# Kernel tuning notes

Hardware: AMD Instinct MI355X
Metric: run time of the kernel (lower is better)

## Reference

```python
import jax, jax.numpy as jnp
import numpy as np
from jax import lax
from jax.scipy.special import logsumexp

NUM_BINS = 1001          # num_bins
K = 127                  # num_quantized_bins = 2**(8-1) - 1 (signed int8, non-narrow)
HALF = NUM_BINS // 2     # 500
EPS = 1e-4               # smoothing_eps
NEG = -1e30              # mask value for logsumexp


def setup_inputs() -> dict:
    key = jax.random.key(0)
    x = jax.random.normal(key, (8, 4096, 1024), dtype=jnp.float32)
    return {"x": x}


def _smooth_logits(v, valid, L):
    # Faithful to smooth_normalize_distribution: hist += eps*is_zeros - eps1*n_nonzeros
    is_zero = valid & (v == 0)
    n_zeros = jnp.sum(is_zero).astype(jnp.float32)
    n_nz = L.astype(jnp.float32) - n_zeros
    eps1 = EPS * n_zeros / jnp.maximum(n_nz, 1.0)
    logits = v + EPS * is_zero.astype(jnp.float32) - eps1 * n_nz
    return logits, n_nz


def reference(x):
    absmax = jnp.max(jnp.abs(x))
    edges = jnp.linspace(-absmax, absmax, NUM_BINS + 1)           # hist_edges, len 1002
    counts, _ = jnp.histogram(x.ravel(), bins=edges)
    hist = lax.stop_gradient(counts.astype(jnp.float32))          # torch.histc(...).int()
    csum = jnp.concatenate([jnp.zeros(1, jnp.float32), jnp.cumsum(hist)])  # exclusive prefix
    total = csum[-1]
    hist_pad = jnp.concatenate([hist, jnp.zeros(NUM_BINS, jnp.float32)])
    k = jnp.arange(NUM_BINS)

    def per_candidate(i):
        start = HALF - i
        stop = HALF + i + 1
        L = 2 * i + 1                          # length of sliced histogram
        valid = k < L
        sliced = lax.dynamic_slice(hist_pad, (start,), (NUM_BINS,))  # first L entries valid
        left = csum[start]                     # sum(hist[:start])
        right = total - csum[stop]             # sum(hist[stop:])
        p = sliced.at[0].add(left).at[L - 1].add(right)
        m = L // K                             # num_merged_bins
        seg = jnp.minimum(k // m, K - 1)       # merged-bin id per position (remainder -> last)
        seg_v = jnp.where(valid, seg, K)       # dump invalid into extra segment
        qb = jax.ops.segment_sum(jnp.where(valid, sliced, 0.0), seg_v, num_segments=K + 1)[:K]
        nz = valid & (sliced != 0)
        # norm for bin j counts nonzeros in its range; last bin uses stop=-1 (excludes k=L-1)
        cnt_mask = nz & (k != L - 1)
        norms = jax.ops.segment_sum(cnt_mask.astype(jnp.float32), seg_v, num_segments=K + 1)[:K]
        nk = norms[seg]
        qbk = qb[seg]
        # q[start:stop] = qb[j]/norm where norm != 0; k=L-1 never assigned; q[sliced==0]=0
        q = jnp.where(nz & (k != L - 1) & (nk > 0), qbk / jnp.maximum(nk, 1.0), 0.0)

        p_log, _ = _smooth_logits(p, valid, L)
        q_log, n_nz_q = _smooth_logits(q, valid, L)
        lZp = logsumexp(jnp.where(valid, p_log, NEG))
        lZq = logsumexp(jnp.where(valid, q_log, NEG))
        lp = p_log - lZp
        lq = q_log - lZq
        probs = jnp.where(valid, jnp.exp(lp), 0.0)
        kl = jnp.sum(probs * (lp - lq) * valid)
        kl = jnp.where(n_nz_q > 0, kl, jnp.inf)  # q all-zero -> divergence = inf
        return edges[stop], kl

    ivals = jnp.arange(K // 2, HALF + 1)        # i = 63 .. 500 (438 candidates)
    thresholds, divergence = jax.vmap(per_candidate)(ivals)
    return thresholds[jnp.argmin(divergence)]
```

## Files before the change

### kernel.cpp

```cpp
#include <hip/hip_runtime.h>
#include <math.h>

#define NBINS 1001
#define KQ 127
#define HALFB 500
#define SEPS 1e-4f
#define NCAND 438
#define IMIN 63
#define PMAXN 2048

typedef float vfloat4 __attribute__((ext_vector_type(4)));

static __device__ __forceinline__ vfloat4 ntload4(const vfloat4* p) {
    return __builtin_nontemporal_load(p);
}


static __device__ __forceinline__ float edge_at(int j, float stepv, float negabs) {
    return __fadd_rn(__fmul_rn((float)j, stepv), negabs);
}

static __device__ __forceinline__ void blockSum2(double& a, double& b, double* s8) {
    for (int s = 32; s > 0; s >>= 1) {
        a += __shfl_down(a, s, 64);
        b += __shfl_down(b, s, 64);
    }
    const int w = threadIdx.x >> 6, l = threadIdx.x & 63;
    __syncthreads();
    if (l == 0) { s8[w] = a; s8[4 + w] = b; }
    __syncthreads();
    a = (s8[0] + s8[1]) + (s8[2] + s8[3]);
    b = (s8[4] + s8[5]) + (s8[6] + s8[7]);
}

static __device__ __forceinline__ double blockSum1(double a, double* s8) {
    for (int s = 32; s > 0; s >>= 1) a += __shfl_down(a, s, 64);
    const int w = threadIdx.x >> 6, l = threadIdx.x & 63;
    __syncthreads();
    if (l == 0) s8[w] = a;
    __syncthreads();
    return (s8[0] + s8[1]) + (s8[2] + s8[3]);
}

static __device__ __forceinline__ void blockMax2(float& a, float& b, double* s8) {
    for (int s = 32; s > 0; s >>= 1) {
        a = fmaxf(a, __shfl_down(a, s, 64));
        b = fmaxf(b, __shfl_down(b, s, 64));
    }
    const int w = threadIdx.x >> 6, l = threadIdx.x & 63;
    __syncthreads();
    if (l == 0) { s8[w] = (double)a; s8[4 + w] = (double)b; }
    __syncthreads();
    a = fmaxf(fmaxf((float)s8[0], (float)s8[1]), fmaxf((float)s8[2], (float)s8[3]));
    b = fmaxf(fmaxf((float)s8[4], (float)s8[5]), fmaxf((float)s8[6], (float)s8[7]));
}


__global__ __launch_bounds__(256) void absmax_kernel(const float* __restrict__ x,
                                                     long long n,
                                                     float* __restrict__ pmax,
                                                     unsigned int* __restrict__ ws_u) {
    __shared__ float red[256];
    if (blockIdx.x == 0) {
        for (int t = threadIdx.x; t < NBINS; t += 256) ws_u[4 + t] = 0u;
        if (threadIdx.x == 0) ws_u[0] = 0u;
    }
    float m = 0.f;
    long long idx = (long long)blockIdx.x * blockDim.x + threadIdx.x;
    long long stride = (long long)gridDim.x * blockDim.x;
    const vfloat4* x4 = (const vfloat4*)x;
    long long n4 = n >> 2;
    long long i = idx;
    for (; i + stride < n4; i += 2 * stride) {
        vfloat4 a = ntload4(&x4[i]);
        vfloat4 b = ntload4(&x4[i + stride]);
        m = fmaxf(m, fmaxf(fmaxf(fabsf(a.x), fabsf(a.y)), fmaxf(fabsf(a.z), fabsf(a.w))));
        m = fmaxf(m, fmaxf(fmaxf(fabsf(b.x), fabsf(b.y)), fmaxf(fabsf(b.z), fabsf(b.w))));
    }
    for (; i < n4; i += stride) {
        vfloat4 a = ntload4(&x4[i]);
        m = fmaxf(m, fmaxf(fmaxf(fabsf(a.x), fabsf(a.y)), fmaxf(fabsf(a.z), fabsf(a.w))));
    }
    for (long long j = (n4 << 2) + idx; j < n; j += stride)
        m = fmaxf(m, fabsf(x[j]));
    red[threadIdx.x] = m;
    __syncthreads();
    for (int s = 128; s > 0; s >>= 1) {
        if (threadIdx.x < s) red[threadIdx.x] = fmaxf(red[threadIdx.x], red[threadIdx.x + s]);
        __syncthreads();
    }
    if (threadIdx.x == 0) pmax[blockIdx.x] = red[0];
}

static __device__ __forceinline__ void bin_one(float v, float inv, float cofs,
                                               float stepv, float negabs,
                                               unsigned int* __restrict__ sh) {
    float t = __builtin_fmaf(v, inv, cofs);
    int b = (int)t;
    b = b < 0 ? 0 : (b > NBINS - 1 ? NBINS - 1 : b);
    float e_lo = edge_at(b, stepv, negabs);
    float e_hi = edge_at(b + 1, stepv, negabs);
    int up = (v >= e_hi) & (b < NBINS - 1);
    int dn = (v < e_lo) & (b > 0);
    b += up - dn;
    unsigned int addr = (unsigned int)(unsigned long long)(&sh[b]);
    asm volatile("ds_add_u32 %0, %1" :: "v"(addr), "v"(1u));
}

__global__ __launch_bounds__(256) void hist_kernel(const float* __restrict__ x,
                                                   long long n,
                                                   const float* __restrict__ pmax,
                                                   unsigned int* __restrict__ hist,
                                                   unsigned int* __restrict__ absmax_bits) {
    __shared__ unsigned int sh[4 * NBINS];
    __shared__ float redm[256];
    {
        float m = 0.f;
        for (int t = threadIdx.x; t < PMAXN; t += 256) m = fmaxf(m, pmax[t]);
        redm[threadIdx.x] = m;
        __syncthreads();
        for (int s = 128; s > 0; s >>= 1) {
            if (threadIdx.x < s) redm[threadIdx.x] = fmaxf(redm[threadIdx.x], redm[threadIdx.x + s]);
            __syncthreads();
        }
    }
    float absmax = redm[0];
    if (blockIdx.x == 0 && threadIdx.x == 0) *absmax_bits = __float_as_uint(absmax);

    for (int i = threadIdx.x; i < 4 * NBINS; i += blockDim.x) sh[i] = 0u;
    __syncthreads();
    unsigned int* mysh = sh + (threadIdx.x >> 6) * NBINS;

    float negabs = -absmax;
    float stepv = __fdiv_rn(__fmul_rn(2.0f, absmax), 1001.0f);
    float inv = __fdiv_rn(1001.0f, __fmul_rn(2.0f, absmax));
    float cofs = __fmul_rn(absmax, inv);

    long long idx = (long long)blockIdx.x * blockDim.x + threadIdx.x;
    long long stride = (long long)gridDim.x * blockDim.x;
    const vfloat4* x4 = (const vfloat4*)x;
    long long n4 = n >> 2;
    long long i = idx;
    for (; i + stride < n4; i += 2 * stride) {
        vfloat4 a = ntload4(&x4[i]);
        vfloat4 b = ntload4(&x4[i + stride]);
        bin_one(a.x, inv, cofs, stepv, negabs, mysh);
        bin_one(a.y, inv, cofs, stepv, negabs, mysh);
        bin_one(a.z, inv, cofs, stepv, negabs, mysh);
        bin_one(a.w, inv, cofs, stepv, negabs, mysh);
        bin_one(b.x, inv, cofs, stepv, negabs, mysh);
        bin_one(b.y, inv, cofs, stepv, negabs, mysh);
        bin_one(b.z, inv, cofs, stepv, negabs, mysh);
        bin_one(b.w, inv, cofs, stepv, negabs, mysh);
    }
    for (; i < n4; i += stride) {
        vfloat4 a = ntload4(&x4[i]);
        bin_one(a.x, inv, cofs, stepv, negabs, mysh);
        bin_one(a.y, inv, cofs, stepv, negabs, mysh);
        bin_one(a.z, inv, cofs, stepv, negabs, mysh);
        bin_one(a.w, inv, cofs, stepv, negabs, mysh);
    }
    for (long long j = (n4 << 2) + idx; j < n; j += stride)
        bin_one(x[j], inv, cofs, stepv, negabs, mysh);

    asm volatile("s_waitcnt lgkmcnt(0)" ::: "memory");
    __syncthreads();
    for (int i2 = threadIdx.x; i2 < NBINS; i2 += blockDim.x) {
        unsigned int s = sh[i2] + sh[NBINS + i2] + sh[2 * NBINS + i2] + sh[3 * NBINS + i2];
        if (s) atomicAdd(&hist[i2], s);
    }
}

__global__ __launch_bounds__(1024) void scan_kernel(const unsigned int* __restrict__ hist,
                                                    double* __restrict__ csumD,
                                                    int* __restrict__ nzc) {
    __shared__ double sd[1024];
    __shared__ int si[1024];
    int t = threadIdx.x;
    unsigned int h = (t < NBINS) ? hist[t] : 0u;
    sd[t] = (double)((float)h);
    si[t] = (t < NBINS && h != 0u) ? 1 : 0;
    __syncthreads();
    for (int off = 1; off < 1024; off <<= 1) {
        double dv = 0.0; int iv = 0;
        if (t >= off) { dv = sd[t - off]; iv = si[t - off]; }
        __syncthreads();
        sd[t] += dv; si[t] += iv;
        __syncthreads();
    }
    if (t < NBINS) { csumD[t + 1] = sd[t]; nzc[t + 1] = si[t]; }
    if (t == 0) { csumD[0] = 0.0; nzc[0] = 0; }
}

__global__ __launch_bounds__(256) void cand_kernel(const unsigned int* __restrict__ hist,
                                                   const double* __restrict__ csumD,
                                                   const int* __restrict__ nzc,
                                                   float* __restrict__ divg) {
    const int i = IMIN + (int)blockIdx.x;
    const int L = 2 * i + 1;
    const int start = HALFB - i;
    const int stop = start + L;
    const int m = L / KQ;
    const unsigned int magic = (65536u + (unsigned)m - 1u) / (unsigned)m;
    const int tid = threadIdx.x;

    __shared__ float s_h[NBINS];
    __shared__ float s_qb[KQ];
    __shared__ float s_nkf[KQ];
    __shared__ double s8[8];

    for (int k = tid; k < NBINS; k += 256) s_h[k] = (float)hist[k];

    double csS = csumD[start], csE = csumD[stop], total = csumD[NBINS];
    float left = (float)csS;
    float right = (float)(total - csE);
    float s0 = (float)hist[start];
    float sL1 = (float)hist[stop - 1];
    int nzwin = nzc[stop] - nzc[start];
    int nnzq = nzwin - ((sL1 != 0.f) ? 1 : 0);
    int nzeros_s = L - nzwin;
    float n_zeros_p = (float)(nzeros_s
                              - ((s0 == 0.f && csS > 0.0) ? 1 : 0)
                              - ((sL1 == 0.f && (total - csE) > 0.0) ? 1 : 0));

    float n_nz_p = (float)L - n_zeros_p;
    float eps1p = SEPS * n_zeros_p / fmaxf(n_nz_p, 1.0f);
    float cp = eps1p * n_nz_p;

    float n_zeros_q = (float)L - (float)nnzq;
    float n_nz_qf = (float)L - n_zeros_q;
    float eps1q = SEPS * n_zeros_q / fmaxf(n_nz_qf, 1.0f);
    float cq = eps1q * n_nz_qf;

    if (tid < KQ) {
        int lo = start + tid * m;
        int hi = (tid == KQ - 1) ? stop : (lo + m);
        s_qb[tid] = (float)(csumD[hi] - csumD[lo]);
        int nrm = (nzc[hi] - nzc[lo]) - ((tid == KQ - 1 && sL1 != 0.f) ? 1 : 0);
        s_nkf[tid] = (float)nrm;
    }
    __syncthreads();

    float ppre[4], qpre[4];
    float maxpp = -INFINITY, maxqq = -INFINITY;
#pragma unroll
    for (int j = 0; j < 4; ++j) {
        int k = tid + 256 * j;
        ppre[j] = 0.f; qpre[j] = 0.f;
        if (k < L) {
            float s = s_h[start + k];
            float p = s;
            if (k == 0) p += left;
            if (k == L - 1) p += right;
            float pp = (p == 0.f) ? SEPS : p;
            int seg = (int)(((unsigned)k * magic) >> 16);
            if (seg > KQ - 1) seg = KQ - 1;
            float qv = 0.f;
            if (s != 0.f && k != L - 1) {
                float nk = s_nkf[seg];
                if (nk > 0.f) qv = s_qb[seg] / nk;
            }
            float qq = (qv == 0.f) ? SEPS : qv;
            ppre[j] = pp; qpre[j] = qq;
            maxpp = fmaxf(maxpp, pp);
            maxqq = fmaxf(maxqq, qq);
        }
    }
    blockMax2(maxpp, maxqq, s8);
    float maxplog = maxpp - cp;
    float maxqlog = maxqq - cq;

    double sp = 0.0, sq = 0.0;
#pragma unroll
    for (int j = 0; j < 4; ++j) {
        int k = tid + 256 * j;
        if (k < L) {
            sp += (double)expf((ppre[j] - cp) - maxplog);
            sq += (double)expf((qpre[j] - cq) - maxqlog);
        }
    }
    blockSum2(sp, sq, s8);
    float lZp = maxplog + (float)log(sp);
    float lZq = maxqlog + (float)log(sq);

    double kll = 0.0;
#pragma unroll
    for (int j = 0; j < 4; ++j) {
        int k = tid + 256 * j;
        if (k < L) {
            float pl = ppre[j] - cp;
            float ql = qpre[j] - cq;
            float lp = pl - lZp;
            float lq = ql - lZq;
            kll += (double)(expf(lp) * (lp - lq));
        }
    }
    double KL = blockSum1(kll, s8);
    if (tid == 0) divg[blockIdx.x] = (nnzq > 0) ? (float)KL : INFINITY;
}

__global__ void argmin_kernel(const float* __restrict__ divg,
                              const unsigned int* __restrict__ absmax_bits,
                              float* __restrict__ out) {
    __shared__ float vals[512];
    __shared__ int idxs[512];
    int tid = threadIdx.x;
    vals[tid] = (tid < NCAND) ? divg[tid] : INFINITY;
    idxs[tid] = tid;
    __syncthreads();
    for (int s = 256; s > 0; s >>= 1) {
        if (tid < s) {
            float a = vals[tid], b = vals[tid + s];
            int ia = idxs[tid], ib = idxs[tid + s];
            if (b < a || (b == a && ib < ia)) { vals[tid] = b; idxs[tid] = ib; }
        }
        __syncthreads();
    }
    if (tid == 0) {
        int i = IMIN + idxs[0];
        int stop = HALFB + i + 1;
        float absmax = __uint_as_float(*absmax_bits);
        float stepv = __fdiv_rn(__fmul_rn(2.0f, absmax), 1001.0f);
        out[0] = __fadd_rn(__fmul_rn((float)stop, stepv), -absmax);
    }
}

extern "C" void kernel_launch(void* const* d_in, const int* in_sizes, int n_in,
                              void* d_out, int out_size, void* d_ws, size_t ws_size,
                              hipStream_t stream) {
    const float* x = (const float*)d_in[0];
    long long n = (long long)in_sizes[0];

    unsigned int* ws_u = (unsigned int*)d_ws;
    unsigned int* absmax_bits = ws_u;
    unsigned int* hist = ws_u + 4;
    float* divg = (float*)(ws_u + 1028);
    double* csumD = (double*)(ws_u + 1536);
    int* nzc = (int*)(ws_u + 3544);
    float* pmax = (float*)(ws_u + 4608);
    float* out = (float*)d_out;

    hipLaunchKernelGGL(absmax_kernel, dim3(PMAXN), dim3(256), 0, stream, x, n, pmax, ws_u);
    hipLaunchKernelGGL(hist_kernel, dim3(1024), dim3(256), 0, stream, x, n, pmax, hist, absmax_bits);
    hipLaunchKernelGGL(scan_kernel, dim3(1), dim3(1024), 0, stream, hist, csumD, nzc);
    hipLaunchKernelGGL(cand_kernel, dim3(NCAND), dim3(256), 0, stream, hist, csumD, nzc, divg);
    hipLaunchKernelGGL(argmin_kernel, dim3(1), dim3(512), 0, stream, divg, absmax_bits, out);
}
```

Baseline: 238.8 us.

## Fuse scan into histogram tail and argmin into candidate kernel via last-block atomics

The separate scan and argmin kernels are removed. The last histogram block, detected with an atomic counter, now runs the prefix scan. Each candidate block folds its KL value into a packed 64-bit atomicMin key, and the last block to finish writes the threshold. This cuts two kernel launches and their serialization gaps, at the cost of threadfences and atomic counters that must be reset each call.

```diff
diff --git a/kernel.cpp b/kernel.cpp
--- a/kernel.cpp
+++ b/kernel.cpp
@@ -8,6 +8,7 @@
 #define NCAND 438
 #define IMIN 63
 #define PMAXN 2048
+#define HISTG 1024
 
 typedef float vfloat4 __attribute__((ext_vector_type(4)));
 
@@ -63,7 +64,12 @@
     __shared__ float red[256];
     if (blockIdx.x == 0) {
         for (int t = threadIdx.x; t < NBINS; t += 256) ws_u[4 + t] = 0u;
-        if (threadIdx.x == 0) ws_u[0] = 0u;
+        if (threadIdx.x == 0) {
+            ws_u[0] = 0u;
+            ws_u[1008] = 0u;
+            ws_u[1012] = 0u;
+            *(unsigned long long*)(ws_u + 2) = ~0ULL;
+        }
     }
     float m = 0.f;
     long long idx = (long long)blockIdx.x * blockDim.x + threadIdx.x;
@@ -110,10 +116,14 @@
 __global__ __launch_bounds__(256) void hist_kernel(const float* __restrict__ x,
                                                    long long n,
                                                    const float* __restrict__ pmax,
-                                                   unsigned int* __restrict__ hist,
-                                                   unsigned int* __restrict__ absmax_bits) {
-    __shared__ unsigned int sh[4 * NBINS];
+                                                   unsigned int* __restrict__ ws_u,
+                                                   double* __restrict__ csumD,
+                                                   int* __restrict__ nzc) {
+    __shared__ __align__(16) unsigned int sh[4 * NBINS];
     __shared__ float redm[256];
+    __shared__ unsigned int lastFlag;
+    unsigned int* hist = ws_u + 4;
+
     {
         float m = 0.f;
         for (int t = threadIdx.x; t < PMAXN; t += 256) m = fmaxf(m, pmax[t]);
@@ -125,7 +135,7 @@
         }
     }
     float absmax = redm[0];
-    if (blockIdx.x == 0 && threadIdx.x == 0) *absmax_bits = __float_as_uint(absmax);
+    if (blockIdx.x == 0 && threadIdx.x == 0) ws_u[0] = __float_as_uint(absmax);
 
     for (int i = threadIdx.x; i < 4 * NBINS; i += blockDim.x) sh[i] = 0u;
     __syncthreads();
@@ -169,33 +179,53 @@
         unsigned int s = sh[i2] + sh[NBINS + i2] + sh[2 * NBINS + i2] + sh[3 * NBINS + i2];
         if (s) atomicAdd(&hist[i2], s);
     }
-}
-
-__global__ __launch_bounds__(1024) void scan_kernel(const unsigned int* __restrict__ hist,
-                                                    double* __restrict__ csumD,
-                                                    int* __restrict__ nzc) {
-    __shared__ double sd[1024];
-    __shared__ int si[1024];
-    int t = threadIdx.x;
-    unsigned int h = (t < NBINS) ? hist[t] : 0u;
-    sd[t] = (double)((float)h);
-    si[t] = (t < NBINS && h != 0u) ? 1 : 0;
-    __syncthreads();
-    for (int off = 1; off < 1024; off <<= 1) {
-        double dv = 0.0; int iv = 0;
-        if (t >= off) { dv = sd[t - off]; iv = si[t - off]; }
+
+    __threadfence();
+    if (threadIdx.x == 0)
+        lastFlag = (atomicAdd(&ws_u[1008], 1u) == (unsigned)gridDim.x - 1u) ? 1u : 0u;
+    __syncthreads();
+    if (lastFlag) {
+        double* sd = (double*)sh;
+        int* si = (int*)(sh + 2048);
+        const int tid = threadIdx.x;
+#pragma unroll
+        for (int j = 0; j < 4; ++j) {
+            int k = tid + 256 * j;
+            unsigned int h = (k < NBINS) ? atomicAdd(&hist[k], 0u) : 0u;
+            sd[k] = (double)((float)h);
+            si[k] = (k < NBINS && h != 0u) ? 1 : 0;
+        }
         __syncthreads();
-        sd[t] += dv; si[t] += iv;
-        __syncthreads();
-    }
-    if (t < NBINS) { csumD[t + 1] = sd[t]; nzc[t + 1] = si[t]; }
-    if (t == 0) { csumD[0] = 0.0; nzc[0] = 0; }
-}
-
-__global__ __launch_bounds__(256) void cand_kernel(const unsigned int* __restrict__ hist,
-                                                   const double* __restrict__ csumD,
+        for (int off = 1; off < 1024; off <<= 1) {
+            double dv[4]; int iv[4];
+#pragma unroll
+            for (int j = 0; j < 4; ++j) {
+                int k = tid + 256 * j;
+                dv[j] = (k >= off) ? sd[k - off] : 0.0;
+                iv[j] = (k >= off) ? si[k - off] : 0;
+            }
+            __syncthreads();
+#pragma unroll
+            for (int j = 0; j < 4; ++j) {
+                int k = tid + 256 * j;
+                sd[k] += dv[j]; si[k] += iv[j];
+            }
+            __syncthreads();
+        }
+#pragma unroll
+        for (int j = 0; j < 4; ++j) {
+            int k = tid + 256 * j;
+            if (k < NBINS) { csumD[k + 1] = sd[k]; nzc[k + 1] = si[k]; }
+        }
+        if (tid == 0) { csumD[0] = 0.0; nzc[0] = 0; }
+    }
+}
+
+__global__ __launch_bounds__(256) void cand_kernel(const double* __restrict__ csumD,
                                                    const int* __restrict__ nzc,
-                                                   float* __restrict__ divg) {
+                                                   unsigned int* __restrict__ ws_u,
+                                                   float* __restrict__ out) {
+    const unsigned int* hist = ws_u + 4;
     const int i = IMIN + (int)blockIdx.x;
     const int L = 2 * i + 1;
     const int start = HALFB - i;
@@ -296,32 +326,25 @@
         }
     }
     double KL = blockSum1(kll, s8);
-    if (tid == 0) divg[blockIdx.x] = (nnzq > 0) ? (float)KL : INFINITY;
-}
-
-__global__ void argmin_kernel(const float* __restrict__ divg,
-                              const unsigned int* __restrict__ absmax_bits,
-                              float* __restrict__ out) {
-    __shared__ float vals[512];
-    __shared__ int idxs[512];
-    int tid = threadIdx.x;
-    vals[tid] = (tid < NCAND) ? divg[tid] : INFINITY;
-    idxs[tid] = tid;
-    __syncthreads();
-    for (int s = 256; s > 0; s >>= 1) {
-        if (tid < s) {
-            float a = vals[tid], b = vals[tid + s];
-            int ia = idxs[tid], ib = idxs[tid + s];
-            if (b < a || (b == a && ib < ia)) { vals[tid] = b; idxs[tid] = ib; }
-        }
-        __syncthreads();
-    }
+
     if (tid == 0) {
-        int i = IMIN + idxs[0];
-        int stop = HALFB + i + 1;
-        float absmax = __uint_as_float(*absmax_bits);
-        float stepv = __fdiv_rn(__fmul_rn(2.0f, absmax), 1001.0f);
-        out[0] = __fadd_rn(__fmul_rn((float)stop, stepv), -absmax);
+        float kl = (nnzq > 0) ? (float)KL : INFINITY;
+        unsigned int u = __float_as_uint(kl);
+        u = (u & 0x80000000u) ? ~u : (u | 0x80000000u);
+        unsigned long long key = ((unsigned long long)u << 16) | (unsigned int)blockIdx.x;
+        unsigned long long* packed = (unsigned long long*)(ws_u + 2);
+        atomicMin(packed, key);
+        __threadfence();
+        unsigned int prev = atomicAdd(&ws_u[1012], 1u);
+        if (prev == NCAND - 1) {
+            unsigned long long win = atomicAdd(packed, 0ULL);
+            int widx = (int)(win & 0xFFFFull);
+            int wi = IMIN + widx;
+            int wstop = HALFB + wi + 1;
+            float absmax = __uint_as_float(ws_u[0]);
+            float stepv = __fdiv_rn(__fmul_rn(2.0f, absmax), 1001.0f);
+            out[0] = __fadd_rn(__fmul_rn((float)wstop, stepv), -absmax);
+        }
     }
 }
 
@@ -332,17 +355,12 @@
     long long n = (long long)in_sizes[0];
 
     unsigned int* ws_u = (unsigned int*)d_ws;
-    unsigned int* absmax_bits = ws_u;
-    unsigned int* hist = ws_u + 4;
-    float* divg = (float*)(ws_u + 1028);
     double* csumD = (double*)(ws_u + 1536);
     int* nzc = (int*)(ws_u + 3544);
     float* pmax = (float*)(ws_u + 4608);
     float* out = (float*)d_out;
 
     hipLaunchKernelGGL(absmax_kernel, dim3(PMAXN), dim3(256), 0, stream, x, n, pmax, ws_u);
-    hipLaunchKernelGGL(hist_kernel, dim3(1024), dim3(256), 0, stream, x, n, pmax, hist, absmax_bits);
-    hipLaunchKernelGGL(scan_kernel, dim3(1), dim3(1024), 0, stream, hist, csumD, nzc);
-    hipLaunchKernelGGL(cand_kernel, dim3(NCAND), dim3(256), 0, stream, hist, csumD, nzc, divg);
-    hipLaunchKernelGGL(argmin_kernel, dim3(1), dim3(512), 0, stream, divg, absmax_bits, out);
-}
+    hipLaunchKernelGGL(hist_kernel, dim3(HISTG), dim3(256), 0, stream, x, n, pmax, ws_u, csumD, nzc);
+    hipLaunchKernelGGL(cand_kernel, dim3(NCAND), dim3(256), 0, stream, csumD, nzc, ws_u, out);
+}
```

New measurement: 336.6 us. 41.0% more time.
